# Performance work log

Hardware: AMD Instinct MI355X
Metric: run time of the kernel (lower is better)

## Reference

```python
import jax, jax.numpy as jnp
import numpy as np

B, S, D = 4, 2048, 128


def setup_inputs() -> dict:
    key = jax.random.key(0)
    kq, kk, kv = jax.random.split(key, 3)
    query = jax.random.normal(kq, (B, S, D), dtype=jnp.float32)
    key_t = jax.random.normal(kk, (B, S, D), dtype=jnp.float32)
    value = jax.random.normal(kv, (B, S, D), dtype=jnp.float32)
    return {"query": query, "key": key_t, "value": value}


def reference(query, key, value):
    # Raw dot-general attention: contract only the last dim, NO batch dims,
    # so scores have shape [B, Sq, B, Sk] (cross-batch attention).
    scores = jnp.einsum('aqd,bkd->aqbk', query, key)  # [B,S,B,S]
    # softmax over the trailing half of the dims (axes 2 and 3 jointly)
    attn = jax.nn.softmax(scores, axis=(2, 3))
    # Dropout: train=False -> deterministic no-op.
    # Second dot_general contracts trailing (B,Sk) of attn with leading (B,Sk) of value.
    y = jnp.einsum('aqbk,bkd->aqd', attn, value)  # [B,S,D]
    return y
```

## Files before the change

### kernel.cpp

```cpp
#include <hip/hip_runtime.h>
#include <hip/hip_bf16.h>
#include <string.h>

#define NROWS 8192
#define DH    128
#define G     8
#define KPG   1024
#define NIT   (KPG / 64)
#define LOG2E 1.44269504088896340736f
#define MSCALED (56.0f * LOG2E)

typedef __attribute__((ext_vector_type(8)))  short    short8;
typedef __attribute__((ext_vector_type(16))) float    floatx16;
typedef __attribute__((ext_vector_type(4)))  unsigned short us4;
typedef __attribute__((ext_vector_type(8)))  _Float16 half8;
typedef __attribute__((ext_vector_type(4)))  _Float16 half4;

#define MFMA_BF32(a, b, c)  __builtin_amdgcn_mfma_f32_32x32x16_bf16((a), (b), (c), 0, 0, 0)
#define MFMA_F16W(a, b, c)  __builtin_amdgcn_mfma_f32_32x32x16_f16((a), (b), (c), 0, 0, 0)

__device__ __forceinline__ unsigned short f32_to_bf16(float f) {
    union { float f; unsigned u; } v; v.f = f;
    unsigned u = v.u + 0x7FFFu + ((v.u >> 16) & 1u);
    return (unsigned short)(u >> 16);
}
__device__ __forceinline__ float bf16_to_f32(unsigned short h) {
    union { unsigned u; float f; } v; v.u = ((unsigned)h) << 16;
    return v.f;
}
__device__ __forceinline__ float fast_exp2(float x) {
    float r; asm("v_exp_f32 %0, %1" : "=v"(r) : "v"(x)); return r;
}
__device__ __forceinline__ void async_ld16(const void* g, void* lds) {
    __builtin_amdgcn_global_load_lds(
        (const __attribute__((address_space(1))) unsigned int*)g,
        (__attribute__((address_space(3))) unsigned int*)lds, 16, 0, 0);
}

__global__ void prep_kernel(const float* __restrict__ Q, const float* __restrict__ K,
                            const float* __restrict__ V,
                            _Float16* __restrict__ Qf, unsigned short* __restrict__ KV) {
    int bid = blockIdx.x;
    if (bid < 1024) {
        int i = bid * 1024 + threadIdx.x * 4;
        float4 q = *(const float4*)(Q + i);
        half4 o = {(_Float16)q.x, (_Float16)q.y, (_Float16)q.z, (_Float16)q.w};
        *(half4*)(Qf + i) = o;
        return;
    }
    if (bid < 1152) {
        int B = bid - 1024;
        const float* Ksrc = K + (size_t)B * 64 * DH;
        unsigned short* dst = KV + (size_t)B * 16384;
#pragma unroll
        for (int j = 0; j < 4; j++) {
            int ch = j * 256 + threadIdx.x;
            int seg = ch >> 6;
            int within = ch & 63;
            int l31 = within >> 1, h = within & 1;
            int c = seg >> 1, mt = seg & 1;
            const float* src = Ksrc + (size_t)(mt * 32 + l31) * DH + c * 16 + h * 8;
            float4 a = *(const float4*)src;
            float4 b = *(const float4*)(src + 4);
            half8 o = {(_Float16)a.x, (_Float16)a.y, (_Float16)a.z, (_Float16)a.w,
                       (_Float16)b.x, (_Float16)b.y, (_Float16)b.z, (_Float16)b.w};
            *(half8*)(dst + seg * 512 + within * 8) = o;
        }
        return;
    }
    int B = bid - 1152;
    __shared__ unsigned short tile[64][132];
    const float* Vsrc = V + (size_t)B * 64 * DH;
    {
        int row = threadIdx.x >> 2;
        int cb0 = (threadIdx.x & 3) * 32;
#pragma unroll
        for (int j = 0; j < 8; j++) {
            float4 v = *(const float4*)(Vsrc + (size_t)row * DH + cb0 + j * 4);
            tile[row][cb0 + j * 4 + 0] = f32_to_bf16(v.x);
            tile[row][cb0 + j * 4 + 1] = f32_to_bf16(v.y);
            tile[row][cb0 + j * 4 + 2] = f32_to_bf16(v.z);
            tile[row][cb0 + j * 4 + 3] = f32_to_bf16(v.w);
        }
    }
    __syncthreads();
    unsigned short* dstv = KV + (size_t)B * 16384 + 16 * 512;
#pragma unroll
    for (int j = 0; j < 4; j++) {
        int ch = j * 256 + threadIdx.x;
        int seg = ch >> 6;
        int within = ch & 63;
        int rr = within >> 1, h = within & 1;
        int t = seg >> 2, mt = (seg >> 1) & 1, sp = seg & 1;
        int d = t * 32 + rr;
        short8 o;
#pragma unroll
        for (int jj = 0; jj < 8; jj++) {
            int p = mt * 32 + sp * 16 + h * 8 + jj;
            int ar = (p & ~12) | ((p & 8) >> 1) | ((p & 4) << 1);
            o[jj] = tile[ar][d];
        }
        *(short8*)(dstv + seg * 512 + within * 8) = o;
    }
}

__launch_bounds__(256, 2)
__global__ void attn_kernel(const _Float16* __restrict__ Qf,
                            const unsigned short* __restrict__ KV,
                            unsigned short* __restrict__ Opart,
                            float* __restrict__ lsum) {
    __shared__ __align__(16) unsigned short kvbuf[2][32 * 512];

    const int lane = threadIdx.x & 63;
    const int wave = threadIdx.x >> 6;
    const int g    = blockIdx.x & 7;
    const int qt   = blockIdx.x >> 3;
    const int l31  = lane & 31;
    const int h    = lane >> 5;
    const int qrow0 = qt * 128 + wave * 32;

    half8 qf[8];
    {
        const half8* ph = (const half8*)(Qf + (size_t)(qrow0 + l31) * DH + h * 8);
#pragma unroll
        for (int c = 0; c < 8; c++) qf[c] = ph[c * 2];
    }

    floatx16 Oacc[4];
#pragma unroll
    for (int t = 0; t < 4; t++)
#pragma unroll
        for (int e = 0; e < 16; e++) Oacc[t][e] = 0.f;
    float lacc = 0.f;

    const unsigned short* pb = KV + (size_t)(g * 16) * 16384 + lane * 8;
    auto stage = [&](int buf) {
        unsigned short* dst = kvbuf[buf];
#pragma unroll
        for (int j = 0; j < 8; j++) {
            int s = wave + 4 * j;
            async_ld16(pb + s * 512, dst + s * 512);
        }
        pb += 16384;
    };

    const int fo = l31 * 16 + h * 8;

    stage(0);
    for (int it = 0; it < NIT; ++it) {
        __syncthreads();
        if (it + 1 < NIT) stage((it + 1) & 1);

        const unsigned short* cb = kvbuf[it & 1];

        floatx16 S0, S1;
#pragma unroll
        for (int e = 0; e < 16; e++) { S0[e] = 0.f; S1[e] = 0.f; }
#pragma unroll
        for (int c = 0; c < 8; c++) {
            half8 a0 = *(const half8*)(cb + (2 * c) * 512 + fo);
            half8 a1 = *(const half8*)(cb + (2 * c + 1) * 512 + fo);
            S0 = MFMA_F16W(a0, qf[c], S0);
            S1 = MFMA_F16W(a1, qf[c], S1);
        }

        unsigned p0[2][4], p1[2][4];
        auto expack = [&](const floatx16& S, unsigned (&pp)[2][4]) {
#pragma unroll
            for (int sp = 0; sp < 2; sp++)
#pragma unroll
                for (int e = 0; e < 4; e++) {
                    float pa = fast_exp2(__builtin_fmaf(S[8 * sp + 2 * e],     LOG2E, -MSCALED));
                    float pb2 = fast_exp2(__builtin_fmaf(S[8 * sp + 2 * e + 1], LOG2E, -MSCALED));
                    lacc += pa; lacc += pb2;
                    __hip_bfloat162 pk = __float22bfloat162_rn(float2{pa, pb2});
                    unsigned u; memcpy(&u, &pk, 4);
                    pp[sp][e] = u;
                }
        };
        auto pv = [&](const unsigned (&pp)[2][4], int mt) {
#pragma unroll
            for (int sp = 0; sp < 2; sp++) {
                union { unsigned u[4]; short8 s8; } bp;
#pragma unroll
                for (int e = 0; e < 4; e++) bp.u[e] = pp[sp][e];
#pragma unroll
                for (int t = 0; t < 4; t++) {
                    short8 vf = *(const short8*)(cb + (16 + t * 4 + mt * 2 + sp) * 512 + fo);
                    Oacc[t] = MFMA_BF32(vf, bp.s8, Oacc[t]);
                }
            }
        };
        expack(S0, p0);
        pv(p0, 0);
        expack(S1, p1);
        pv(p1, 1);
    }

    unsigned short* op = Opart + ((size_t)g * NROWS + qrow0 + l31) * DH;
#pragma unroll
    for (int t = 0; t < 4; t++)
#pragma unroll
        for (int rg = 0; rg < 4; rg++) {
            us4 w;
#pragma unroll
            for (int e = 0; e < 4; e++) w[e] = f32_to_bf16(Oacc[t][4 * rg + e]);
            *(us4*)(op + 32 * t + 8 * rg + 4 * h) = w;
        }
    lacc += __shfl_xor(lacc, 32);
    if (h == 0) lsum[(size_t)g * NROWS + qrow0 + l31] = lacc;
}

__global__ void merge_kernel(const unsigned short* __restrict__ Opart,
                             const float* __restrict__ lsum, float* __restrict__ out) {
    int t = blockIdx.x * 256 + threadIdx.x;
    int base = t * 8;
    int q = base >> 7;
    float L = 0.f;
#pragma unroll
    for (int g = 0; g < G; g++) L += lsum[(size_t)g * NROWS + q];
    float acc[8] = {0.f, 0.f, 0.f, 0.f, 0.f, 0.f, 0.f, 0.f};
#pragma unroll
    for (int g = 0; g < G; g++) {
        short8 v = *(const short8*)(Opart + (size_t)g * NROWS * DH + base);
#pragma unroll
        for (int j = 0; j < 8; j++) acc[j] += bf16_to_f32((unsigned short)v[j]);
    }
    float inv = 1.0f / L;
    float4 o0 = {acc[0] * inv, acc[1] * inv, acc[2] * inv, acc[3] * inv};
    float4 o1 = {acc[4] * inv, acc[5] * inv, acc[6] * inv, acc[7] * inv};
    *(float4*)(out + base) = o0;
    *(float4*)(out + base + 4) = o1;
}

extern "C" void kernel_launch(void* const* d_in, const int* in_sizes, int n_in,
                              void* d_out, int out_size, void* d_ws, size_t ws_size,
                              hipStream_t stream) {
    const float* Q = (const float*)d_in[0];
    const float* K = (const float*)d_in[1];
    const float* V = (const float*)d_in[2];
    float* out = (float*)d_out;

    char* ws = (char*)d_ws;
    _Float16* Qf = (_Float16*)ws;
    unsigned short* KV = (unsigned short*)(ws + (size_t)NROWS * DH * 2);
    char* p = ws + (size_t)NROWS * DH * 2 + (size_t)128 * 16384 * 2;
    unsigned short* Opart = (unsigned short*)p;
    float* lsum = (float*)(p + (size_t)G * NROWS * DH * sizeof(unsigned short));

    hipLaunchKernelGGL(prep_kernel, dim3(1024 + 128 + 128), dim3(256), 0, stream,
                       Q, K, V, Qf, KV);
    hipLaunchKernelGGL(attn_kernel, dim3((NROWS / 128) * G), dim3(256), 0, stream,
                       Qf, KV, Opart, lsum);
    hipLaunchKernelGGL(merge_kernel, dim3(NROWS * DH / (256 * 8)), dim3(256), 0, stream,
                       Opart, lsum, out);
}
```

Baseline: 112.8 us.

## Split keys into 16 groups with 32-key tiles and raise occupancy

Doubles the key split to 16 groups and processes 32 keys per iteration instead of 64. The K/V packed layout is rebuilt per 32-key block, so each iteration needs half the LDS buffer and a single score accumulator. Launch bounds now allow 4 blocks per CU, and s_setprio is raised around the MFMA sections. The goals are more resident waves to hide latency and more blocks to fill the CUs. In exchange, the merge reads twice as many bf16 partials and each iteration runs more barrier syncs.

```diff
diff --git a/kernel.cpp b/kernel.cpp
--- a/kernel.cpp
+++ b/kernel.cpp
@@ -4,9 +4,11 @@
 
 #define NROWS 8192
 #define DH    128
-#define G     8
-#define KPG   1024
-#define NIT   (KPG / 64)
+#define G     16
+#define KPG   (NROWS / G)
+#define NIT   (KPG / 32)
+#define SEGS  16
+#define B32U  (SEGS * 512)
 #define LOG2E 1.44269504088896340736f
 #define MSCALED (56.0f * LOG2E)
 
@@ -51,20 +53,21 @@
     if (bid < 1152) {
         int B = bid - 1024;
         const float* Ksrc = K + (size_t)B * 64 * DH;
-        unsigned short* dst = KV + (size_t)B * 16384;
+        unsigned short* dst = KV + (size_t)(2 * B) * B32U;
 #pragma unroll
         for (int j = 0; j < 4; j++) {
             int ch = j * 256 + threadIdx.x;
-            int seg = ch >> 6;
-            int within = ch & 63;
-            int l31 = within >> 1, h = within & 1;
-            int c = seg >> 1, mt = seg & 1;
+            int mt = ch >> 9;
+            int rem = ch & 511;
+            int c = rem >> 6;
+            int within = rem & 63;
+            int h = within >> 5, l31 = within & 31;
             const float* src = Ksrc + (size_t)(mt * 32 + l31) * DH + c * 16 + h * 8;
             float4 a = *(const float4*)src;
             float4 b = *(const float4*)(src + 4);
             half8 o = {(_Float16)a.x, (_Float16)a.y, (_Float16)a.z, (_Float16)a.w,
                        (_Float16)b.x, (_Float16)b.y, (_Float16)b.z, (_Float16)b.w};
-            *(half8*)(dst + seg * 512 + within * 8) = o;
+            *(half8*)(dst + (size_t)mt * B32U + c * 512 + within * 8) = o;
         }
         return;
     }
@@ -84,14 +87,16 @@
         }
     }
     __syncthreads();
-    unsigned short* dstv = KV + (size_t)B * 16384 + 16 * 512;
+    unsigned short* dstv = KV + (size_t)(2 * B) * B32U + 8 * 512;
 #pragma unroll
     for (int j = 0; j < 4; j++) {
         int ch = j * 256 + threadIdx.x;
-        int seg = ch >> 6;
-        int within = ch & 63;
-        int rr = within >> 1, h = within & 1;
-        int t = seg >> 2, mt = (seg >> 1) & 1, sp = seg & 1;
+        int mt = ch >> 9;
+        int rem = ch & 511;
+        int seg = rem >> 6;
+        int within = rem & 63;
+        int h = within >> 5, rr = within & 31;
+        int t = seg >> 1, sp = seg & 1;
         int d = t * 32 + rr;
         short8 o;
 #pragma unroll
@@ -100,21 +105,21 @@
             int ar = (p & ~12) | ((p & 8) >> 1) | ((p & 4) << 1);
             o[jj] = tile[ar][d];
         }
-        *(short8*)(dstv + seg * 512 + within * 8) = o;
-    }
-}
-
-__launch_bounds__(256, 2)
+        *(short8*)(dstv + (size_t)mt * B32U + seg * 512 + within * 8) = o;
+    }
+}
+
+__launch_bounds__(256, 4)
 __global__ void attn_kernel(const _Float16* __restrict__ Qf,
                             const unsigned short* __restrict__ KV,
                             unsigned short* __restrict__ Opart,
                             float* __restrict__ lsum) {
-    __shared__ __align__(16) unsigned short kvbuf[2][32 * 512];
+    __shared__ __align__(16) unsigned short kvbuf[2][SEGS * 512];
 
     const int lane = threadIdx.x & 63;
     const int wave = threadIdx.x >> 6;
-    const int g    = blockIdx.x & 7;
-    const int qt   = blockIdx.x >> 3;
+    const int g    = blockIdx.x & (G - 1);
+    const int qt   = blockIdx.x / G;
     const int l31  = lane & 31;
     const int h    = lane >> 5;
     const int qrow0 = qt * 128 + wave * 32;
@@ -131,20 +136,20 @@
     for (int t = 0; t < 4; t++)
 #pragma unroll
         for (int e = 0; e < 16; e++) Oacc[t][e] = 0.f;
-    float lacc = 0.f;
-
-    const unsigned short* pb = KV + (size_t)(g * 16) * 16384 + lane * 8;
+    float la0 = 0.f, la1 = 0.f;
+
+    const unsigned short* pb = KV + (size_t)(g * NIT) * B32U + lane * 8;
     auto stage = [&](int buf) {
         unsigned short* dst = kvbuf[buf];
 #pragma unroll
-        for (int j = 0; j < 8; j++) {
+        for (int j = 0; j < 4; j++) {
             int s = wave + 4 * j;
             async_ld16(pb + s * 512, dst + s * 512);
         }
-        pb += 16384;
+        pb += B32U;
     };
 
-    const int fo = l31 * 16 + h * 8;
+    const int fo = lane * 8;
 
     stage(0);
     for (int it = 0; it < NIT; ++it) {
@@ -153,48 +158,39 @@
 
         const unsigned short* cb = kvbuf[it & 1];
 
-        floatx16 S0, S1;
-#pragma unroll
-        for (int e = 0; e < 16; e++) { S0[e] = 0.f; S1[e] = 0.f; }
+        floatx16 S;
+#pragma unroll
+        for (int e = 0; e < 16; e++) S[e] = 0.f;
+        __builtin_amdgcn_s_setprio(1);
 #pragma unroll
         for (int c = 0; c < 8; c++) {
-            half8 a0 = *(const half8*)(cb + (2 * c) * 512 + fo);
-            half8 a1 = *(const half8*)(cb + (2 * c + 1) * 512 + fo);
-            S0 = MFMA_F16W(a0, qf[c], S0);
-            S1 = MFMA_F16W(a1, qf[c], S1);
-        }
-
-        unsigned p0[2][4], p1[2][4];
-        auto expack = [&](const floatx16& S, unsigned (&pp)[2][4]) {
-#pragma unroll
-            for (int sp = 0; sp < 2; sp++)
-#pragma unroll
-                for (int e = 0; e < 4; e++) {
-                    float pa = fast_exp2(__builtin_fmaf(S[8 * sp + 2 * e],     LOG2E, -MSCALED));
-                    float pb2 = fast_exp2(__builtin_fmaf(S[8 * sp + 2 * e + 1], LOG2E, -MSCALED));
-                    lacc += pa; lacc += pb2;
-                    __hip_bfloat162 pk = __float22bfloat162_rn(float2{pa, pb2});
-                    unsigned u; memcpy(&u, &pk, 4);
-                    pp[sp][e] = u;
-                }
-        };
-        auto pv = [&](const unsigned (&pp)[2][4], int mt) {
-#pragma unroll
-            for (int sp = 0; sp < 2; sp++) {
-                union { unsigned u[4]; short8 s8; } bp;
-#pragma unroll
-                for (int e = 0; e < 4; e++) bp.u[e] = pp[sp][e];
-#pragma unroll
-                for (int t = 0; t < 4; t++) {
-                    short8 vf = *(const short8*)(cb + (16 + t * 4 + mt * 2 + sp) * 512 + fo);
-                    Oacc[t] = MFMA_BF32(vf, bp.s8, Oacc[t]);
-                }
+            half8 a = *(const half8*)(cb + c * 512 + fo);
+            S = MFMA_F16W(a, qf[c], S);
+        }
+        __builtin_amdgcn_s_setprio(0);
+
+#pragma unroll
+        for (int sp = 0; sp < 2; sp++) {
+            union { unsigned u[4]; short8 s8; } bp;
+            float lad = 0.f;
+#pragma unroll
+            for (int e = 0; e < 4; e++) {
+                float pa  = fast_exp2(__builtin_fmaf(S[8 * sp + 2 * e],     LOG2E, -MSCALED));
+                float pb2 = fast_exp2(__builtin_fmaf(S[8 * sp + 2 * e + 1], LOG2E, -MSCALED));
+                lad += pa; lad += pb2;
+                __hip_bfloat162 pk = __float22bfloat162_rn(float2{pa, pb2});
+                unsigned u; memcpy(&u, &pk, 4);
+                bp.u[e] = u;
             }
-        };
-        expack(S0, p0);
-        pv(p0, 0);
-        expack(S1, p1);
-        pv(p1, 1);
+            if (sp == 0) la0 += lad; else la1 += lad;
+            __builtin_amdgcn_s_setprio(1);
+#pragma unroll
+            for (int t = 0; t < 4; t++) {
+                short8 vf = *(const short8*)(cb + (8 + t * 2 + sp) * 512 + fo);
+                Oacc[t] = MFMA_BF32(vf, bp.s8, Oacc[t]);
+            }
+            __builtin_amdgcn_s_setprio(0);
+        }
     }
 
     unsigned short* op = Opart + ((size_t)g * NROWS + qrow0 + l31) * DH;
@@ -207,6 +203,7 @@
             for (int e = 0; e < 4; e++) w[e] = f32_to_bf16(Oacc[t][4 * rg + e]);
             *(us4*)(op + 32 * t + 8 * rg + 4 * h) = w;
         }
+    float lacc = la0 + la1;
     lacc += __shfl_xor(lacc, 32);
     if (h == 0) lsum[(size_t)g * NROWS + qrow0 + l31] = lacc;
 }
@@ -244,7 +241,7 @@
     char* ws = (char*)d_ws;
     _Float16* Qf = (_Float16*)ws;
     unsigned short* KV = (unsigned short*)(ws + (size_t)NROWS * DH * 2);
-    char* p = ws + (size_t)NROWS * DH * 2 + (size_t)128 * 16384 * 2;
+    char* p = ws + (size_t)NROWS * DH * 2 + (size_t)(NROWS / 32) * B32U * 2;
     unsigned short* Opart = (unsigned short*)p;
     float* lsum = (float*)(p + (size_t)G * NROWS * DH * sizeof(unsigned short));
 
```

New measurement: 126.6 us. 1.12x slower.
